# Performance work log

Hardware: AMD Instinct MI355X
Metric: run time of the kernel (lower is better)

Reference implementation:

```python
import jax, jax.numpy as jnp
import numpy as np

DEPTH = 9            # perfect binary tree depth (root=level 0, leaves=level DEPTH)
N_TREES = 128
H = 256              # h_size == x_size (ndata['h'] init uses x_size)
NPT = 2 ** (DEPTH + 1) - 1   # 1023 nodes per tree
N = N_TREES * NPT            # 130944 total nodes


def _levels():
    """Static per-level (node, left-child, right-child) global index arrays."""
    base = np.arange(N_TREES, dtype=np.int64)[:, None] * NPT
    out = []
    for l in range(DEPTH + 1):
        loc = np.arange(2 ** l - 1, 2 ** (l + 1) - 1, dtype=np.int64)
        nodes = (base + loc[None, :]).reshape(-1)
        if l < DEPTH:
            cl = (base + (2 * loc + 1)[None, :]).reshape(-1)
            cr = (base + (2 * loc + 2)[None, :]).reshape(-1)
        else:
            cl = cr = None
        out.append((jnp.asarray(nodes),
                    None if cl is None else jnp.asarray(cl),
                    None if cr is None else jnp.asarray(cr)))
    return out


def setup_inputs() -> dict:
    key = jax.random.key(0)
    ks = jax.random.split(key, 10)
    s = lambda d: 1.0 / np.sqrt(d)
    return {
        "wordid": jax.random.randint(ks[0], (N,), 0, 32000),
        "mask":   jax.random.randint(ks[1], (N,), 0, 2),
        "emb":    jax.random.normal(ks[2], (32000, H), jnp.float32) * 0.02,
        "W_iou":  jax.random.normal(ks[3], (H, 3 * H), jnp.float32) * s(H),
        "U_iou":  jax.random.normal(ks[4], (2 * H, 3 * H), jnp.float32) * s(2 * H),
        "U_f_w":  jax.random.normal(ks[5], (2 * H, 2 * H), jnp.float32) * s(2 * H),
        "U_f_b":  jax.random.normal(ks[6], (2 * H,), jnp.float32) * 0.01,
        "b_iou":  jax.random.normal(ks[7], (3 * H,), jnp.float32) * 0.01,
        "lin_w":  jax.random.normal(ks[8], (H, 4), jnp.float32) * s(H),
        "lin_b":  jax.random.normal(ks[9], (4,), jnp.float32) * 0.01,
    }


def _apply_node(iou, b_iou, c_in, mh_in):
    i, o, u = jnp.split(iou + b_iou, 3, axis=1)
    i, o, u = jax.nn.sigmoid(i), jax.nn.sigmoid(o), jnp.tanh(u)
    c = i * u + c_in
    h = o * jnp.tanh(c)
    return h, c, jnp.maximum(h, mh_in)


def reference(wordid, mask, emb, W_iou, U_iou, U_f_w, U_f_b, b_iou, lin_w, lin_b):
    levels = _levels()
    x = emb[wordid * mask]                                  # [N, H]
    iou0 = (x @ W_iou) * mask[:, None].astype(x.dtype)      # leaf/pre-set iou [N, 3H]

    h = jnp.zeros((N, H), x.dtype)
    c = jnp.zeros((N, H), x.dtype)
    mh = jnp.zeros((N, H), x.dtype)

    # leaves: no incoming messages -> apply with preset iou, c=0, max_h=0
    li, _, _ = levels[DEPTH]
    hh, cc, mm = _apply_node(iou0[li], b_iou, 0.0, 0.0)
    h, c, mh = h.at[li].set(hh), c.at[li].set(cc), mh.at[li].set(mm)

    # internal levels, bottom-up (DGL prop_nodes_topo)
    for l in range(DEPTH - 1, -1, -1):
        ni, cl, cr = levels[l]
        h_cat = jnp.concatenate([h[cl], h[cr]], axis=1)     # [M, 2H]
        f = jax.nn.sigmoid(h_cat @ U_f_w + U_f_b)           # [M, 2H]
        fl, fr = jnp.split(f, 2, axis=1)
        c_red = fl * c[cl] + fr * c[cr]
        mh_red = jnp.maximum(mh[cl], mh[cr])
        iou = h_cat @ U_iou                                  # overwrites preset iou
        hh, cc, mm = _apply_node(iou, b_iou, c_red, mh_red)
        h, c, mh = h.at[ni].set(hh), c.at[ni].set(cc), mh.at[ni].set(mm)

    return (h + mh) @ lin_w + lin_b                         # logits [N, num_classes]
```

## Files before the change

kernel.cpp:

```cpp
#include <hip/hip_runtime.h>
#include <hip/hip_bf16.h>


#define NTREES 128
#define NPT    1023
#define HS     256
#define NNODES (NTREES * NPT)

typedef __hip_bfloat16 bf16;
typedef unsigned short us8 __attribute__((ext_vector_type(8)));
typedef unsigned short us4 __attribute__((ext_vector_type(4)));
typedef short bf16x8 __attribute__((ext_vector_type(8)));
typedef float f32x4 __attribute__((ext_vector_type(4)));

typedef __attribute__((address_space(1))) const void gvoid;
typedef __attribute__((address_space(3))) void svoid;
#define GLD16(gp, lp) \
    __builtin_amdgcn_global_load_lds((gvoid*)(gp), (svoid*)(lp), 16, 0, 0)

__device__ __forceinline__ float bits2f(unsigned short b) {
    return __uint_as_float(((unsigned)b) << 16);
}
__device__ __forceinline__ float ld_bf(const bf16* p) {
    return bits2f(*reinterpret_cast<const unsigned short*>(p));
}
__device__ __forceinline__ unsigned short f2bits(float x) {
    bf16 h = __float2bfloat16(x);
    return *reinterpret_cast<unsigned short*>(&h);
}
__device__ __forceinline__ float fsigm(float x) {
    return __builtin_amdgcn_rcpf(1.0f + __expf(-x));
}
__device__ __forceinline__ float ftanh(float x) {
    return 1.0f - 2.0f * __builtin_amdgcn_rcpf(1.0f + __expf(2.0f * x));
}

#define WT_ELEMS (768 * 256)
#define UT_ELEMS (1280 * 512)

__global__ __launch_bounds__(256) void prep_w(
    const float* __restrict__ W_iou, const float* __restrict__ U_f_w,
    const float* __restrict__ U_iou, bf16* __restrict__ Wt, bf16* __restrict__ Ut)
{
    const int i = blockIdx.x * 256 + threadIdx.x;
    if (i < WT_ELEMS) {
        const int n = i >> 8, k = i & 255;
        Wt[i] = __float2bfloat16(W_iou[k * 768 + n]);
    } else if (i < WT_ELEMS + UT_ELEMS) {
        const int j = i - WT_ELEMS;
        const int n = j >> 9, k = j & 511;
        const float v = (n < 512) ? U_f_w[k * 512 + n] : U_iou[k * 768 + (n - 512)];
        Ut[j] = __float2bfloat16(v);
    }
}

__global__ __launch_bounds__(256) void leaf_fused(
    const int* __restrict__ wordid, const int* __restrict__ mask,
    const float* __restrict__ emb, const bf16* __restrict__ Wt,
    const float* __restrict__ b_iou,
    bf16* __restrict__ h_s, bf16* __restrict__ c_s, bf16* __restrict__ mh_s,
    bf16* __restrict__ s_full, const int tree0)
{
    __shared__ __align__(16) short a_s[128 * 32];
    __shared__ __align__(16) short b_s[96 * 32];
    const int t    = threadIdx.x;
    const int bm0  = blockIdx.x * 128;
    const int c0   = blockIdx.y * 32;
    const int lane = t & 63, wave = t >> 6;

    const int k8t = (t & 3) * 8;
    const float* aptr[2];
    int amask[2];
    #pragma unroll
    for (int p = 0; p < 2; ++p) {
        const int row  = p * 64 + (t >> 2);
        const int gr   = tree0 * 512 + bm0 + row;
        const int node = (gr >> 9) * NPT + 511 + (gr & 511);
        amask[p] = mask[node];
        aptr[p]  = emb + (long)wordid[node] * HS + k8t;
    }

    const int l4a = lane >> 2, k8 = (lane & 3) * 8;
    const int bCnt = (wave < 3) ? 2 : 0;
    const int bStart = wave * 2;
    const bf16* bSrc[2];
    #pragma unroll
    for (int q = 0; q < 2; ++q) {
        int rb = (bStart + q) * 16 + l4a;
        if (rb > 95) rb = 95;
        const int g = rb >> 5, jl = rb & 31;
        bSrc[q] = Wt + (long)(g * 256 + c0 + jl) * 256 + k8;
    }

    const int wr = wave >> 1, wc = wave & 1;
    const int fr = lane & 15, l4 = lane >> 4;

    f32x4 acc[4][3];
    #pragma unroll
    for (int i = 0; i < 4; ++i)
        #pragma unroll
        for (int g = 0; g < 3; ++g) acc[i][g] = (f32x4){0.f, 0.f, 0.f, 0.f};

    for (int kt = 0; kt < 256; kt += 32) {
        __syncthreads();
        #pragma unroll
        for (int q = 0; q < 2; ++q)
            if (q < bCnt) GLD16(bSrc[q] + kt, &b_s[(bStart + q) * 512]);
        #pragma unroll
        for (int p = 0; p < 2; ++p) {
            short tmp[8];
            if (amask[p]) {
                const float4 v0 = *(const float4*)(aptr[p] + kt);
                const float4 v1 = *(const float4*)(aptr[p] + kt + 4);
                tmp[0] = (short)f2bits(v0.x); tmp[1] = (short)f2bits(v0.y);
                tmp[2] = (short)f2bits(v0.z); tmp[3] = (short)f2bits(v0.w);
                tmp[4] = (short)f2bits(v1.x); tmp[5] = (short)f2bits(v1.y);
                tmp[6] = (short)f2bits(v1.z); tmp[7] = (short)f2bits(v1.w);
            } else {
                #pragma unroll
                for (int q = 0; q < 8; ++q) tmp[q] = 0;
            }
            *(us8*)&a_s[p * 2048 + t * 8] = *(us8*)&tmp[0];
        }
        __syncthreads();
        bf16x8 af[4], bg[3];
        #pragma unroll
        for (int i = 0; i < 4; ++i)
            af[i] = *(const bf16x8*)&a_s[(wr * 64 + i * 16 + fr) * 32 + l4 * 8];
        #pragma unroll
        for (int g = 0; g < 3; ++g)
            bg[g] = *(const bf16x8*)&b_s[(g * 32 + wc * 16 + fr) * 32 + l4 * 8];
        #pragma unroll
        for (int i = 0; i < 4; ++i)
            #pragma unroll
            for (int g = 0; g < 3; ++g)
                acc[i][g] = __builtin_amdgcn_mfma_f32_16x16x32_bf16(
                    af[i], bg[g], acc[i][g], 0, 0, 0);
    }

    const int j  = c0 + wc * 16 + fr;
    const float bi = b_iou[j], bo = b_iou[256 + j], bu = b_iou[512 + j];
    #pragma unroll
    for (int i = 0; i < 4; ++i) {
        #pragma unroll
        for (int q = 0; q < 4; ++q) {
            const int r    = bm0 + wr * 64 + i * 16 + l4 * 4 + q;
            const int gr   = tree0 * 512 + r;
            const int node = (gr >> 9) * NPT + 511 + (gr & 511);
            const float iv = fsigm(acc[i][0][q] + bi);
            const float ov = fsigm(acc[i][1][q] + bo);
            const float uv = ftanh(acc[i][2][q] + bu);
            const float cv  = iv * uv;
            const float hv  = ov * ftanh(cv);
            const float mhv = fmaxf(hv, 0.0f);
            const long o = (long)r * HS + j;
            h_s[o]  = __float2bfloat16(hv);
            c_s[o]  = __float2bfloat16(cv);
            mh_s[o] = __float2bfloat16(mhv);
            s_full[(long)node * HS + j] = __float2bfloat16(hv + mhv);
        }
    }
}

__global__ __launch_bounds__(256) void level_fused(
    const bf16* __restrict__ h_child, const bf16* __restrict__ c_c,
    const bf16* __restrict__ mh_c, const bf16* __restrict__ Ut,
    const float* __restrict__ U_f_b, const float* __restrict__ b_iou,
    bf16* __restrict__ h_p, bf16* __restrict__ c_p, bf16* __restrict__ mh_p,
    bf16* __restrict__ s_full, const int lvl, const int M, const int tree0)
{
    __shared__ __align__(16) short a_s[128 * 32];
    __shared__ __align__(16) short b_s[160 * 32];
    const int t    = threadIdx.x;
    const int bm0  = blockIdx.x * 128;
    const int c0   = blockIdx.y * 32;
    const int lane = t & 63, wave = t >> 6;

    const int l4a = lane >> 2, k8 = (lane & 3) * 8;

    const bf16* aSrc[2];
    #pragma unroll
    for (int q = 0; q < 2; ++q) {
        int p = bm0 + wave * 32 + q * 16 + l4a;
        if (p >= M) p = M - 1;
        const int tl  = p >> lvl;
        const int idx = p & ((1 << lvl) - 1);
        const int cls = tl * (2 << lvl) + 2 * idx;
        aSrc[q] = h_child + (long)cls * HS + k8;
    }
    const int bCnt   = (wave < 2) ? 3 : 2;
    const int bStart = (wave < 2) ? wave * 3 : 6 + (wave - 2) * 2;
    const bf16* bSrc[3];
    #pragma unroll
    for (int q = 0; q < 3; ++q) {
        int rb = (bStart + q) * 16 + l4a;
        if (rb > 159) rb = 159;
        const int g = rb >> 5, jl = rb & 31;
        bSrc[q] = Ut + (long)(g * 256 + c0 + jl) * 512 + k8;
    }

    const int wr = wave >> 1, wc = wave & 1;
    const int fr = lane & 15, l4 = lane >> 4;

    f32x4 acc[4][5];
    #pragma unroll
    for (int i = 0; i < 4; ++i)
        #pragma unroll
        for (int g = 0; g < 5; ++g) acc[i][g] = (f32x4){0.f, 0.f, 0.f, 0.f};

    for (int kt = 0; kt < 512; kt += 32) {
        __syncthreads();
        #pragma unroll
        for (int q = 0; q < 2; ++q)
            GLD16(aSrc[q] + kt, &a_s[(wave * 2 + q) * 512]);
        #pragma unroll
        for (int q = 0; q < 3; ++q)
            if (q < bCnt) GLD16(bSrc[q] + kt, &b_s[(bStart + q) * 512]);
        __syncthreads();
        bf16x8 af[4], bg[5];
        #pragma unroll
        for (int i = 0; i < 4; ++i)
            af[i] = *(const bf16x8*)&a_s[(wr * 64 + i * 16 + fr) * 32 + l4 * 8];
        #pragma unroll
        for (int g = 0; g < 5; ++g)
            bg[g] = *(const bf16x8*)&b_s[(g * 32 + wc * 16 + fr) * 32 + l4 * 8];
        #pragma unroll
        for (int i = 0; i < 4; ++i)
            #pragma unroll
            for (int g = 0; g < 5; ++g)
                acc[i][g] = __builtin_amdgcn_mfma_f32_16x16x32_bf16(
                    af[i], bg[g], acc[i][g], 0, 0, 0);
    }

    const int j = c0 + wc * 16 + fr;
    const float bfl = U_f_b[j], bfr = U_f_b[256 + j];
    const float bi = b_iou[j], bo = b_iou[256 + j], bu = b_iou[512 + j];
    #pragma unroll
    for (int i = 0; i < 4; ++i) {
        #pragma unroll
        for (int q = 0; q < 4; ++q) {
            const int p = bm0 + wr * 64 + i * 16 + l4 * 4 + q;
            if (p < M) {
                const int tl   = p >> lvl;
                const int idx  = p & ((1 << lvl) - 1);
                const int cls  = tl * (2 << lvl) + 2 * idx;
                const int node = (tree0 + tl) * NPT + (1 << lvl) - 1 + idx;
                const float flv = fsigm(acc[i][0][q] + bfl);
                const float frv = fsigm(acc[i][1][q] + bfr);
                const float iv  = fsigm(acc[i][2][q] + bi);
                const float ov  = fsigm(acc[i][3][q] + bo);
                const float uv  = ftanh(acc[i][4][q] + bu);
                const float ccl = ld_bf(c_c  + (long)cls * HS + j);
                const float ccr = ld_bf(c_c  + (long)(cls + 1) * HS + j);
                const float mhl = ld_bf(mh_c + (long)cls * HS + j);
                const float mhr = ld_bf(mh_c + (long)(cls + 1) * HS + j);
                const float cv  = iv * uv + flv * ccl + frv * ccr;
                const float hv  = ov * ftanh(cv);
                const float mhv = fmaxf(hv, fmaxf(mhl, mhr));
                const long o = (long)p * HS + j;
                h_p[o]  = __float2bfloat16(hv);
                c_p[o]  = __float2bfloat16(cv);
                mh_p[o] = __float2bfloat16(mhv);
                s_full[(long)node * HS + j] = __float2bfloat16(hv + mhv);
            }
        }
    }
}

__global__ __launch_bounds__(256) void logits_k(
    const bf16* __restrict__ s_full, const float* __restrict__ lin_w,
    const float* __restrict__ lin_b, float* __restrict__ out)
{
    const int wave = threadIdx.x >> 6, lane = threadIdx.x & 63;
    const int node = blockIdx.x * 4 + wave;
    const int j0   = lane * 4;
    const us4 v = *(const us4*)(s_full + (long)node * HS + j0);
    float p0 = 0.f, p1 = 0.f, p2 = 0.f, p3 = 0.f;
    #pragma unroll
    for (int q = 0; q < 4; ++q) {
        const float s  = bits2f(v[q]);
        const float4 w = *(const float4*)(lin_w + (j0 + q) * 4);
        p0 += s * w.x; p1 += s * w.y; p2 += s * w.z; p3 += s * w.w;
    }
    #pragma unroll
    for (int m = 1; m < 64; m <<= 1) {
        p0 += __shfl_xor(p0, m); p1 += __shfl_xor(p1, m);
        p2 += __shfl_xor(p2, m); p3 += __shfl_xor(p3, m);
    }
    if (lane == 0) {
        float4 r;
        r.x = p0 + lin_b[0]; r.y = p1 + lin_b[1];
        r.z = p2 + lin_b[2]; r.w = p3 + lin_b[3];
        *(float4*)(out + (long)node * 4) = r;
    }
}

extern "C" void kernel_launch(void* const* d_in, const int* in_sizes, int n_in,
                              void* d_out, int out_size, void* d_ws, size_t ws_size,
                              hipStream_t stream) {
    const int*   wordid = (const int*)d_in[0];
    const int*   mask   = (const int*)d_in[1];
    const float* emb    = (const float*)d_in[2];
    const float* W_iou  = (const float*)d_in[3];
    const float* U_iou  = (const float*)d_in[4];
    const float* U_f_w  = (const float*)d_in[5];
    const float* U_f_b  = (const float*)d_in[6];
    const float* b_iou  = (const float*)d_in[7];
    const float* lin_w  = (const float*)d_in[8];
    const float* lin_b  = (const float*)d_in[9];
    float* out = (float*)d_out;

    const size_t wElems = (size_t)WT_ELEMS + UT_ELEMS;
    const size_t sElems = (size_t)NNODES * HS;
    auto need = [&](int T) -> size_t {
        return (wElems + sElems + (size_t)T * 589824) * 2;
    };
    int T = 8;
    const int cands[4] = {128, 64, 32, 16};
    for (int ci = 0; ci < 4; ++ci) {
        if (need(cands[ci]) <= ws_size) { T = cands[ci]; break; }
    }

    bf16* Wt     = (bf16*)d_ws;
    bf16* Ut     = Wt + WT_ELEMS;
    bf16* s_full = Ut + UT_ELEMS;
    const size_t aR = (size_t)T * 512 * HS;
    const size_t bR = (size_t)T * 256 * HS;
    bf16* hA  = s_full + sElems;
    bf16* cA  = hA  + aR;
    bf16* mhA = cA  + aR;
    bf16* hB  = mhA + aR;
    bf16* cB  = hB  + bR;
    bf16* mhB = cB  + bR;

    prep_w<<<(int)((wElems + 255) / 256), 256, 0, stream>>>(
        W_iou, U_f_w, U_iou, Wt, Ut);

    for (int tree0 = 0; tree0 < NTREES; tree0 += T) {
        leaf_fused<<<dim3(T * 512 / 128, 8), 256, 0, stream>>>(
            wordid, mask, emb, Wt, b_iou, hA, cA, mhA, s_full, tree0);
        bool childIsA = true;
        for (int l = 8; l >= 0; --l) {
            bf16 *hc, *cc, *mc, *hp, *cp, *mp;
            if (childIsA) { hc = hA; cc = cA; mc = mhA; hp = hB; cp = cB; mp = mhB; }
            else          { hc = hB; cc = cB; mc = mhB; hp = hA; cp = cA; mp = mhA; }
            const int M = T << l;
            level_fused<<<dim3((M + 127) / 128, 8), 256, 0, stream>>>(
                hc, cc, mc, Ut, U_f_b, b_iou, hp, cp, mp, s_full, l, M, tree0);
            childIsA = !childIsA;
        }
    }
    logits_k<<<NNODES / 4, 256, 0, stream>>>(s_full, lin_w, lin_b, out);
}
```

Before: 453.6 us.

## Double-buffer LDS tiles, interleave c/mh buffers, vectorize epilogue stores

```diff
diff --git a/kernel.cpp b/kernel.cpp
--- a/kernel.cpp
+++ b/kernel.cpp
@@ -20,9 +20,6 @@
 
 __device__ __forceinline__ float bits2f(unsigned short b) {
     return __uint_as_float(((unsigned)b) << 16);
-}
-__device__ __forceinline__ float ld_bf(const bf16* p) {
-    return bits2f(*reinterpret_cast<const unsigned short*>(p));
 }
 __device__ __forceinline__ unsigned short f2bits(float x) {
     bf16 h = __float2bfloat16(x);
@@ -58,11 +55,11 @@
     const int* __restrict__ wordid, const int* __restrict__ mask,
     const float* __restrict__ emb, const bf16* __restrict__ Wt,
     const float* __restrict__ b_iou,
-    bf16* __restrict__ h_s, bf16* __restrict__ c_s, bf16* __restrict__ mh_s,
+    bf16* __restrict__ h_s, bf16* __restrict__ cm_s,
     bf16* __restrict__ s_full, const int tree0)
 {
-    __shared__ __align__(16) short a_s[128 * 32];
-    __shared__ __align__(16) short b_s[96 * 32];
+    __shared__ __align__(16) short a_s[2][128 * 32];
+    __shared__ __align__(16) short b_s[2][96 * 32];
     const int t    = threadIdx.x;
     const int bm0  = blockIdx.x * 128;
     const int c0   = blockIdx.y * 32;
@@ -101,11 +98,12 @@
         #pragma unroll
         for (int g = 0; g < 3; ++g) acc[i][g] = (f32x4){0.f, 0.f, 0.f, 0.f};
 
-    for (int kt = 0; kt < 256; kt += 32) {
-        __syncthreads();
+    auto stageB = [&](int buf, int kt) {
         #pragma unroll
         for (int q = 0; q < 2; ++q)
-            if (q < bCnt) GLD16(bSrc[q] + kt, &b_s[(bStart + q) * 512]);
+            if (q < bCnt) GLD16(bSrc[q] + kt, &b_s[buf][(bStart + q) * 512]);
+    };
+    auto stageA = [&](int buf, int kt) {
         #pragma unroll
         for (int p = 0; p < 2; ++p) {
             short tmp[8];
@@ -120,57 +118,70 @@
                 #pragma unroll
                 for (int q = 0; q < 8; ++q) tmp[q] = 0;
             }
-            *(us8*)&a_s[p * 2048 + t * 8] = *(us8*)&tmp[0];
-        }
-        __syncthreads();
+            *(us8*)&a_s[buf][p * 2048 + t * 8] = *(us8*)&tmp[0];
+        }
+    };
+
+    stageB(0, 0);
+    stageA(0, 0);
+    __syncthreads();
+    int cur = 0;
+    for (int kt = 0; kt < 256; kt += 32) {
+        const int nk = kt + 32;
+        if (nk < 256) { stageB(cur ^ 1, nk); stageA(cur ^ 1, nk); }
         bf16x8 af[4], bg[3];
         #pragma unroll
         for (int i = 0; i < 4; ++i)
-            af[i] = *(const bf16x8*)&a_s[(wr * 64 + i * 16 + fr) * 32 + l4 * 8];
+            af[i] = *(const bf16x8*)&a_s[cur][(wr * 64 + i * 16 + fr) * 32 + l4 * 8];
         #pragma unroll
         for (int g = 0; g < 3; ++g)
-            bg[g] = *(const bf16x8*)&b_s[(g * 32 + wc * 16 + fr) * 32 + l4 * 8];
+            bg[g] = *(const bf16x8*)&b_s[cur][(g * 32 + wc * 16 + fr) * 32 + l4 * 8];
         #pragma unroll
         for (int i = 0; i < 4; ++i)
             #pragma unroll
             for (int g = 0; g < 3; ++g)
                 acc[i][g] = __builtin_amdgcn_mfma_f32_16x16x32_bf16(
-                    af[i], bg[g], acc[i][g], 0, 0, 0);
-    }
-
-    const int j  = c0 + wc * 16 + fr;
-    const float bi = b_iou[j], bo = b_iou[256 + j], bu = b_iou[512 + j];
+                    bg[g], af[i], acc[i][g], 0, 0, 0);
+        __syncthreads();
+        cur ^= 1;
+    }
+
+    const int j0 = c0 + wc * 16 + l4 * 4;
+    const float4 bi4 = *(const float4*)(b_iou + j0);
+    const float4 bo4 = *(const float4*)(b_iou + 256 + j0);
+    const float4 bu4 = *(const float4*)(b_iou + 512 + j0);
     #pragma unroll
     for (int i = 0; i < 4; ++i) {
+        const int r    = bm0 + wr * 64 + i * 16 + fr;
+        const int gr   = tree0 * 512 + r;
+        const int node = (gr >> 9) * NPT + 511 + (gr & 511);
+        us4 sh, ss; us8 scm;
         #pragma unroll
         for (int q = 0; q < 4; ++q) {
-            const int r    = bm0 + wr * 64 + i * 16 + l4 * 4 + q;
-            const int gr   = tree0 * 512 + r;
-            const int node = (gr >> 9) * NPT + 511 + (gr & 511);
-            const float iv = fsigm(acc[i][0][q] + bi);
-            const float ov = fsigm(acc[i][1][q] + bo);
-            const float uv = ftanh(acc[i][2][q] + bu);
+            const float iv = fsigm(acc[i][0][q] + ((const float*)&bi4)[q]);
+            const float ov = fsigm(acc[i][1][q] + ((const float*)&bo4)[q]);
+            const float uv = ftanh(acc[i][2][q] + ((const float*)&bu4)[q]);
             const float cv  = iv * uv;
             const float hv  = ov * ftanh(cv);
             const float mhv = fmaxf(hv, 0.0f);
-            const long o = (long)r * HS + j;
-            h_s[o]  = __float2bfloat16(hv);
-            c_s[o]  = __float2bfloat16(cv);
-            mh_s[o] = __float2bfloat16(mhv);
-            s_full[(long)node * HS + j] = __float2bfloat16(hv + mhv);
-        }
+            sh[q] = f2bits(hv); ss[q] = f2bits(hv + mhv);
+            scm[2 * q] = f2bits(cv); scm[2 * q + 1] = f2bits(mhv);
+        }
+        *(us4*)(h_s + (long)r * HS + j0)        = sh;
+        *(us8*)(cm_s + (long)r * 512 + j0 * 2)  = scm;
+        *(us4*)(s_full + (long)node * HS + j0)  = ss;
     }
 }
 
 __global__ __launch_bounds__(256) void level_fused(
-    const bf16* __restrict__ h_child, const bf16* __restrict__ c_c,
-    const bf16* __restrict__ mh_c, const bf16* __restrict__ Ut,
+    const bf16* __restrict__ h_child, const bf16* __restrict__ cm_c,
+    const bf16* __restrict__ Ut,
     const float* __restrict__ U_f_b, const float* __restrict__ b_iou,
-    bf16* __restrict__ h_p, bf16* __restrict__ c_p, bf16* __restrict__ mh_p,
+    bf16* __restrict__ h_p, bf16* __restrict__ cm_p,
     bf16* __restrict__ s_full, const int lvl, const int M, const int tree0)
 {
-    __shared__ __align__(16) short a_s[128 * 32];
-    __shared__ __align__(16) short b_s[160 * 32];
+    __shared__ __align__(16) short a_s[2][128 * 32];
+    __shared__ __align__(16) short b_s[2][160 * 32];
     const int t    = threadIdx.x;
     const int bm0  = blockIdx.x * 128;
     const int c0   = blockIdx.y * 32;
@@ -208,61 +219,74 @@
         #pragma unroll
         for (int g = 0; g < 5; ++g) acc[i][g] = (f32x4){0.f, 0.f, 0.f, 0.f};
 
+    auto stage = [&](int buf, int kt) {
+        #pragma unroll
+        for (int q = 0; q < 2; ++q)
+            GLD16(aSrc[q] + kt, &a_s[buf][(wave * 2 + q) * 512]);
+        #pragma unroll
+        for (int q = 0; q < 3; ++q)
+            if (q < bCnt) GLD16(bSrc[q] + kt, &b_s[buf][(bStart + q) * 512]);
+    };
+
+    stage(0, 0);
+    __syncthreads();
+    int cur = 0;
     for (int kt = 0; kt < 512; kt += 32) {
-        __syncthreads();
-        #pragma unroll
-        for (int q = 0; q < 2; ++q)
-            GLD16(aSrc[q] + kt, &a_s[(wave * 2 + q) * 512]);
-        #pragma unroll
-        for (int q = 0; q < 3; ++q)
-            if (q < bCnt) GLD16(bSrc[q] + kt, &b_s[(bStart + q) * 512]);
-        __syncthreads();
+        const int nk = kt + 32;
+        if (nk < 512) stage(cur ^ 1, nk);
         bf16x8 af[4], bg[5];
         #pragma unroll
         for (int i = 0; i < 4; ++i)
-            af[i] = *(const bf16x8*)&a_s[(wr * 64 + i * 16 + fr) * 32 + l4 * 8];
+            af[i] = *(const bf16x8*)&a_s[cur][(wr * 64 + i * 16 + fr) * 32 + l4 * 8];
         #pragma unroll
         for (int g = 0; g < 5; ++g)
-            bg[g] = *(const bf16x8*)&b_s[(g * 32 + wc * 16 + fr) * 32 + l4 * 8];
+            bg[g] = *(const bf16x8*)&b_s[cur][(g * 32 + wc * 16 + fr) * 32 + l4 * 8];
         #pragma unroll
         for (int i = 0; i < 4; ++i)
             #pragma unroll
             for (int g = 0; g < 5; ++g)
                 acc[i][g] = __builtin_amdgcn_mfma_f32_16x16x32_bf16(
-                    af[i], bg[g], acc[i][g], 0, 0, 0);
-    }
-
-    const int j = c0 + wc * 16 + fr;
-    const float bfl = U_f_b[j], bfr = U_f_b[256 + j];
-    const float bi = b_iou[j], bo = b_iou[256 + j], bu = b_iou[512 + j];
+                    bg[g], af[i], acc[i][g], 0, 0, 0);
+        __syncthreads();
+        cur ^= 1;
+    }
+
+    const int j0 = c0 + wc * 16 + l4 * 4;
+    const float4 bfl4 = *(const float4*)(U_f_b + j0);
+    const float4 bfr4 = *(const float4*)(U_f_b + 256 + j0);
+    const float4 bi4  = *(const float4*)(b_iou + j0);
+    const float4 bo4  = *(const float4*)(b_iou + 256 + j0);
+    const float4 bu4  = *(const float4*)(b_iou + 512 + j0);
     #pragma unroll
     for (int i = 0; i < 4; ++i) {
+        const int r  = bm0 + wr * 64 + i * 16 + fr;
+        const int rc = r < M ? r : M - 1;
+        const int tl   = rc >> lvl;
+        const int idx  = rc & ((1 << lvl) - 1);
+        const int cls  = tl * (2 << lvl) + 2 * idx;
+        const int node = (tree0 + tl) * NPT + (1 << lvl) - 1 + idx;
+        const us8 cml = *(const us8*)(cm_c + (long)cls * 512 + j0 * 2);
+        const us8 cmr = *(const us8*)(cm_c + (long)(cls + 1) * 512 + j0 * 2);
+        us4 sh, ss; us8 scm;
         #pragma unroll
         for (int q = 0; q < 4; ++q) {
-            const int p = bm0 + wr * 64 + i * 16 + l4 * 4 + q;
-            if (p < M) {
-                const int tl   = p >> lvl;
-                const int idx  = p & ((1 << lvl) - 1);
-                const int cls  = tl * (2 << lvl) + 2 * idx;
-                const int node = (tree0 + tl) * NPT + (1 << lvl) - 1 + idx;
-                const float flv = fsigm(acc[i][0][q] + bfl);
-                const float frv = fsigm(acc[i][1][q] + bfr);
-                const float iv  = fsigm(acc[i][2][q] + bi);
-                const float ov  = fsigm(acc[i][3][q] + bo);
-                const float uv  = ftanh(acc[i][4][q] + bu);
-                const float ccl = ld_bf(c_c  + (long)cls * HS + j);
-                const float ccr = ld_bf(c_c  + (long)(cls + 1) * HS + j);
-                const float mhl = ld_bf(mh_c + (long)cls * HS + j);
-                const float mhr = ld_bf(mh_c + (long)(cls + 1) * HS + j);
-                const float cv  = iv * uv + flv * ccl + frv * ccr;
-                const float hv  = ov * ftanh(cv);
-                const float mhv = fmaxf(hv, fmaxf(mhl, mhr));
-                const long o = (long)p * HS + j;
-                h_p[o]  = __float2bfloat16(hv);
-                c_p[o]  = __float2bfloat16(cv);
-                mh_p[o] = __float2bfloat16(mhv);
-                s_full[(long)node * HS + j] = __float2bfloat16(hv + mhv);
-            }
+            const float flv = fsigm(acc[i][0][q] + ((const float*)&bfl4)[q]);
+            const float frv = fsigm(acc[i][1][q] + ((const float*)&bfr4)[q]);
+            const float iv  = fsigm(acc[i][2][q] + ((const float*)&bi4)[q]);
+            const float ov  = fsigm(acc[i][3][q] + ((const float*)&bo4)[q]);
+            const float uv  = ftanh(acc[i][4][q] + ((const float*)&bu4)[q]);
+            const float ccl = bits2f(cml[2 * q]), mhl = bits2f(cml[2 * q + 1]);
+            const float ccr = bits2f(cmr[2 * q]), mhr = bits2f(cmr[2 * q + 1]);
+            const float cv  = iv * uv + flv * ccl + frv * ccr;
+            const float hv  = ov * ftanh(cv);
+            const float mhv = fmaxf(hv, fmaxf(mhl, mhr));
+            sh[q] = f2bits(hv); ss[q] = f2bits(hv + mhv);
+            scm[2 * q] = f2bits(cv); scm[2 * q + 1] = f2bits(mhv);
+        }
+        if (r < M) {
+            *(us4*)(h_p + (long)r * HS + j0)       = sh;
+            *(us8*)(cm_p + (long)r * 512 + j0 * 2) = scm;
+            *(us4*)(s_full + (long)node * HS + j0) = ss;
         }
     }
 }
@@ -324,29 +348,25 @@
     bf16* Wt     = (bf16*)d_ws;
     bf16* Ut     = Wt + WT_ELEMS;
     bf16* s_full = Ut + UT_ELEMS;
-    const size_t aR = (size_t)T * 512 * HS;
-    const size_t bR = (size_t)T * 256 * HS;
     bf16* hA  = s_full + sElems;
-    bf16* cA  = hA  + aR;
-    bf16* mhA = cA  + aR;
-    bf16* hB  = mhA + aR;
-    bf16* cB  = hB  + bR;
-    bf16* mhB = cB  + bR;
+    bf16* cmA = hA  + (size_t)T * 512 * HS;
+    bf16* hB  = cmA + (size_t)T * 512 * HS * 2;
+    bf16* cmB = hB  + (size_t)T * 256 * HS;
 
     prep_w<<<(int)((wElems + 255) / 256), 256, 0, stream>>>(
         W_iou, U_f_w, U_iou, Wt, Ut);
 
     for (int tree0 = 0; tree0 < NTREES; tree0 += T) {
         leaf_fused<<<dim3(T * 512 / 128, 8), 256, 0, stream>>>(
-            wordid, mask, emb, Wt, b_iou, hA, cA, mhA, s_full, tree0);
+            wordid, mask, emb, Wt, b_iou, hA, cmA, s_full, tree0);
         bool childIsA = true;
         for (int l = 8; l >= 0; --l) {
-            bf16 *hc, *cc, *mc, *hp, *cp, *mp;
-            if (childIsA) { hc = hA; cc = cA; mc = mhA; hp = hB; cp = cB; mp = mhB; }
-            else          { hc = hB; cc = cB; mc = mhB; hp = hA; cp = cA; mp = mhA; }
+            bf16 *hc, *cmc, *hp, *cmp;
+            if (childIsA) { hc = hA; cmc = cmA; hp = hB; cmp = cmB; }
+            else          { hc = hB; cmc = cmB; hp = hA; cmp = cmA; }
             const int M = T << l;
             level_fused<<<dim3((M + 127) / 128, 8), 256, 0, stream>>>(
-                hc, cc, mc, Ut, U_f_b, b_iou, hp, cp, mp, s_full, l, M, tree0);
+                hc, cmc, Ut, U_f_b, b_iou, hp, cmp, s_full, l, M, tree0);
             childIsA = !childIsA;
         }
     }
```

Result: faster. 419.8 us (-7.5%).
